# Optimization experiments

Hardware: AMD Instinct MI355X
Metric: run time of the kernel (lower is better)

## Reference

```python
import jax, jax.numpy as jnp
import numpy as np

B, N, C, H, W = 32, 64, 3, 512, 512
P = 16               # patch_size
NUM_CLASSES = 128


def setup_inputs() -> dict:
    key = jax.random.key(0)
    k1, k2, k3, k4 = jax.random.split(key, 4)
    image = jax.random.normal(k1, (B, C, H, W), dtype=jnp.float32)
    emb = jax.random.normal(k2, (NUM_CLASSES, P * P * 3), dtype=jnp.float32)
    labels = jax.random.randint(k3, (B, N), 0, NUM_CLASSES)
    # precomputed top-left corners; original clamps so corners lie in [0, H-P]
    top_left = jax.random.randint(k4, (B, N, 2), 0, H - P + 1)
    return {"image": image, "emb": emb, "labels": labels, "top_left": top_left}


def reference(image, emb, labels, top_left):
    # gather patches: [B, N, 3, P, P]
    patches = emb[labels].reshape(B, N, 3, P, P)
    # reorder so channel dim trails the advanced-index result dims: [B, N, P, P, 3]
    vals = jnp.transpose(patches, (0, 1, 3, 4, 2))
    bb = jnp.arange(B)[:, None, None, None]                                 # [B,1,1,1]
    rr = top_left[..., 0][:, :, None, None] + jnp.arange(P)[None, None, :, None]  # [B,N,P,1]
    cc = top_left[..., 1][:, :, None, None] + jnp.arange(P)[None, None, None, :]  # [B,N,1,P]
    # scatter-add each patch into the image at its computed offset (overlaps sum)
    return image.at[bb, :, rr, cc].add(vals)
```

## Files before the change

### kernel.cpp

```cpp
#include <hip/hip_runtime.h>
#include <hip/hip_bf16.h>

#define B_   32
#define N_   64
#define C_   3
#define H_   512
#define W_   512
#define P_   16
#define PLANE (H_ * W_)
#define IMG   (C_ * PLANE)

__global__ __launch_bounds__(128)
void ImagePatch_fused_kernel(const float* __restrict__ image,
                             const float* __restrict__ emb,
                             const int*   __restrict__ labels,
                             const int*   __restrict__ top_left,
                             float*       __restrict__ out) {
    __shared__ int s_cnt;
    __shared__ int s_dr[N_];
    __shared__ int s_tc[N_];
    __shared__ int s_lb[N_];

    const int bid = blockIdx.x;
    const int r   = bid & (H_ - 1);
    const int b   = bid >> 9;
    const int tid = threadIdx.x;

    if (tid < 64) {
        const int idx = b * N_ + tid;
        const int tr  = top_left[idx * 2];
        const unsigned dr = (unsigned)(r - tr);
        const bool cover  = dr < P_;
        const unsigned long long m = __ballot(cover);
        if (cover) {
            const int pos = __popcll(m & ((1ull << tid) - 1ull));
            s_dr[pos] = (int)dr;
            s_tc[pos] = top_left[idx * 2 + 1];
            s_lb[pos] = labels[idx];
        }
        if (tid == 0) s_cnt = __popcll(m);
    }
    __syncthreads();

    const int c0 = tid * 4;
    const size_t base = (size_t)b * IMG + (size_t)r * W_ + c0;

    float4 v0 = *(const float4*)(image + base);
    float4 v1 = *(const float4*)(image + base + PLANE);
    float4 v2 = *(const float4*)(image + base + 2 * PLANE);

    const int cnt = s_cnt;
    for (int k = 0; k < cnt; ++k) {
        const int tc = s_tc[k];
        if (c0 + 3 >= tc && c0 < tc + P_) {
            const float* e = emb + s_lb[k] * (C_ * P_ * P_) + s_dr[k] * P_;
            #pragma unroll
            for (int q = 0; q < 4; ++q) {
                const unsigned dc = (unsigned)(c0 + q - tc);
                if (dc < P_) {
                    ((float*)&v0)[q] += e[dc];
                    ((float*)&v1)[q] += e[P_ * P_ + dc];
                    ((float*)&v2)[q] += e[2 * P_ * P_ + dc];
                }
            }
        }
    }

    *(float4*)(out + base)             = v0;
    *(float4*)(out + base + PLANE)     = v1;
    *(float4*)(out + base + 2 * PLANE) = v2;
}

extern "C" void kernel_launch(void* const* d_in, const int* in_sizes, int n_in,
                              void* d_out, int out_size, void* d_ws, size_t ws_size,
                              hipStream_t stream) {
    const float* image    = (const float*)d_in[0];
    const float* emb      = (const float*)d_in[1];
    const int*   labels   = (const int*)d_in[2];
    const int*   top_left = (const int*)d_in[3];
    float*       out      = (float*)d_out;

    const int grid = B_ * H_;
    ImagePatch_fused_kernel<<<grid, 128, 0, stream>>>(image, emb, labels, top_left, out);
}
```

Before: 36.53 us.

## Process 16-row bands per block to amortize patch-list setup

Each block now handles a 16-row band across all three channels with 256 threads, instead of one row with 128 threads. The grid shrinks from 16384 to 1024 blocks, so the per-block top_left/labels scan and barrier are paid once per band rather than once per row. The cost is a larger candidate patch list per band that every thread scans for every element it processes, and fewer blocks to keep the GPU busy. Each thread now loads one channel at a time instead of three planes at once, which lowers memory-level parallelism per thread.

```diff
diff --git a/kernel.cpp b/kernel.cpp
--- a/kernel.cpp
+++ b/kernel.cpp
@@ -7,34 +7,36 @@
 #define H_   512
 #define W_   512
 #define P_   16
+#define BAND 16
 #define PLANE (H_ * W_)
 #define IMG   (C_ * PLANE)
 
-__global__ __launch_bounds__(128)
+typedef float f32x4 __attribute__((ext_vector_type(4)));
+
+__global__ __launch_bounds__(256)
 void ImagePatch_fused_kernel(const float* __restrict__ image,
                              const float* __restrict__ emb,
                              const int*   __restrict__ labels,
                              const int*   __restrict__ top_left,
                              float*       __restrict__ out) {
     __shared__ int s_cnt;
-    __shared__ int s_dr[N_];
+    __shared__ int s_tr[N_];
     __shared__ int s_tc[N_];
     __shared__ int s_lb[N_];
 
     const int bid = blockIdx.x;
-    const int r   = bid & (H_ - 1);
-    const int b   = bid >> 9;
+    const int r0  = (bid & (H_ / BAND - 1)) * BAND;
+    const int b   = bid >> 5;
     const int tid = threadIdx.x;
 
     if (tid < 64) {
         const int idx = b * N_ + tid;
         const int tr  = top_left[idx * 2];
-        const unsigned dr = (unsigned)(r - tr);
-        const bool cover  = dr < P_;
+        const bool cover = (tr + P_ > r0) && (tr < r0 + BAND);
         const unsigned long long m = __ballot(cover);
         if (cover) {
             const int pos = __popcll(m & ((1ull << tid) - 1ull));
-            s_dr[pos] = (int)dr;
+            s_tr[pos] = tr;
             s_tc[pos] = top_left[idx * 2 + 1];
             s_lb[pos] = labels[idx];
         }
@@ -42,33 +44,35 @@
     }
     __syncthreads();
 
-    const int c0 = tid * 4;
-    const size_t base = (size_t)b * IMG + (size_t)r * W_ + c0;
+    const int cnt = s_cnt;
+    const size_t ibase = (size_t)b * IMG + (size_t)r0 * W_;
 
-    float4 v0 = *(const float4*)(image + base);
-    float4 v1 = *(const float4*)(image + base + PLANE);
-    float4 v2 = *(const float4*)(image + base + 2 * PLANE);
+    for (int it = tid; it < BAND * C_ * (W_ / 4); it += 256) {
+        const int col4 = it & 127;
+        const int row  = (it >> 7) & (BAND - 1);
+        const int ch   = it >> 11;
+        const int c0   = col4 * 4;
+        const size_t off = ibase + (size_t)ch * PLANE + (size_t)row * W_ + c0;
 
-    const int cnt = s_cnt;
-    for (int k = 0; k < cnt; ++k) {
-        const int tc = s_tc[k];
-        if (c0 + 3 >= tc && c0 < tc + P_) {
-            const float* e = emb + s_lb[k] * (C_ * P_ * P_) + s_dr[k] * P_;
-            #pragma unroll
-            for (int q = 0; q < 4; ++q) {
-                const unsigned dc = (unsigned)(c0 + q - tc);
-                if (dc < P_) {
-                    ((float*)&v0)[q] += e[dc];
-                    ((float*)&v1)[q] += e[P_ * P_ + dc];
-                    ((float*)&v2)[q] += e[2 * P_ * P_ + dc];
+        f32x4 v = *(const f32x4*)(image + off);
+
+        const int r = r0 + row;
+        for (int k = 0; k < cnt; ++k) {
+            const unsigned dr = (unsigned)(r - s_tr[k]);
+            const int tc = s_tc[k];
+            if (dr < P_ && c0 + 3 >= tc && c0 < tc + P_) {
+                const float* e = emb + s_lb[k] * (C_ * P_ * P_)
+                                     + ch * (P_ * P_) + dr * P_;
+                #pragma unroll
+                for (int q = 0; q < 4; ++q) {
+                    const unsigned dc = (unsigned)(c0 + q - tc);
+                    if (dc < P_) v[q] += e[dc];
                 }
             }
         }
+
+        *(f32x4*)(out + off) = v;
     }
-
-    *(float4*)(out + base)             = v0;
-    *(float4*)(out + base + PLANE)     = v1;
-    *(float4*)(out + base + 2 * PLANE) = v2;
 }
 
 extern "C" void kernel_launch(void* const* d_in, const int* in_sizes, int n_in,
@@ -80,6 +84,6 @@
     const int*   top_left = (const int*)d_in[3];
     float*       out      = (float*)d_out;
 
-    const int grid = B_ * H_;
-    ImagePatch_fused_kernel<<<grid, 128, 0, stream>>>(image, emb, labels, top_left, out);
+    const int grid = B_ * (H_ / BAND);
+    ImagePatch_fused_kernel<<<grid, 256, 0, stream>>>(image, emb, labels, top_left, out);
 }
```

Result: slower. 88.45 us (+142.2%).
